# Performance work log

Hardware: AMD Instinct MI355X
Metric: run time of the kernel (lower is better)

## Reference

```python
import jax, jax.numpy as jnp
import numpy as np
from jax import lax

D_MODEL = 512
N_BLOCKS = 8
VOCAB = 2048
MEL = 80
D_INNER = 2 * D_MODEL      # standard Mamba expand=2
STATE = 16                 # AudioConstants.MAMBA_STATE_DIM
DT_RANK = D_MODEL // 16    # 32
CONV_K = 4                 # causal depthwise conv kernel
B, T = 4, 2048


def setup_inputs() -> dict:
    key = jax.random.key(0)
    ks = jax.random.split(key, 16)
    s = 0.02
    nb = N_BLOCKS
    inp = {
        "feats": jax.random.normal(ks[0], (B, T, MEL), jnp.float32),
        "feat_lens": jax.random.randint(ks[1], (B,), 0, T, jnp.int32),
        # frontend
        "conv1_w": jax.random.normal(ks[2], (D_MODEL, MEL, 3), jnp.float32) * s,
        "conv1_b": jnp.zeros((D_MODEL,), jnp.float32),
        "conv2_w": jax.random.normal(ks[3], (D_MODEL, D_MODEL, 3), jnp.float32) * s,
        "conv2_b": jnp.zeros((D_MODEL,), jnp.float32),
        # stacked per-block Mamba params (leading dim = n_blocks)
        "norm_w": jnp.ones((nb, D_MODEL), jnp.float32),
        "in_proj_w": jax.random.normal(ks[4], (nb, D_MODEL, 2 * D_INNER), jnp.float32) * s,
        "dwconv_w": jax.random.normal(ks[5], (nb, D_INNER, CONV_K), jnp.float32) * s,
        "dwconv_b": jnp.zeros((nb, D_INNER), jnp.float32),
        "x_proj_w": jax.random.normal(ks[6], (nb, D_INNER, DT_RANK + 2 * STATE), jnp.float32) * s,
        "dt_proj_w": jax.random.normal(ks[7], (nb, DT_RANK, D_INNER), jnp.float32) * s,
        "dt_proj_b": jnp.full((nb, D_INNER), -4.6, jnp.float32),  # softplus(-4.6)~0.01
        "A_log": jnp.tile(jnp.log(jnp.arange(1, STATE + 1, dtype=jnp.float32))[None, None, :], (nb, D_INNER, 1)),
        "Dskip": jnp.ones((nb, D_INNER), jnp.float32),
        "out_proj_w": jax.random.normal(ks[8], (nb, D_INNER, D_MODEL), jnp.float32) * s,
        # CTC head
        "head_w": jax.random.normal(ks[9], (D_MODEL, VOCAB), jnp.float32) * s,
        "head_b": jnp.zeros((VOCAB,), jnp.float32),
    }
    return inp


def _conv1d(x, w, b, stride, pad):
    # x: (B, Cin, L), w: (Cout, Cin, K)
    y = lax.conv_general_dilated(x, w, (stride,), [(pad, pad)],
                                 dimension_numbers=("NCH", "OIH", "NCH"))
    return y + b[None, :, None]


def _mamba_layer(x, p):
    nw, ipw, cw, cb, xpw, dpw, dpb, alog, dsk, opw = p
    res = x
    # RMSNorm
    xn = x * lax.rsqrt(jnp.mean(x * x, axis=-1, keepdims=True) + 1e-5) * nw
    xz = xn @ ipw                                # (B, L, 2*di)
    xs, z = jnp.split(xz, 2, axis=-1)
    # causal depthwise conv over time
    xc = jnp.pad(xs.transpose(0, 2, 1), ((0, 0), (0, 0), (CONV_K - 1, 0)))
    xc = lax.conv_general_dilated(xc, cw[:, None, :], (1,), [(0, 0)],
                                  dimension_numbers=("NCH", "OIH", "NCH"),
                                  feature_group_count=D_INNER)
    xs = jax.nn.silu((xc + cb[None, :, None]).transpose(0, 2, 1))  # (B, L, di)
    # input-dependent SSM params
    xdb = xs @ xpw                               # (B, L, dt_rank + 2N)
    dt, Bm, Cm = jnp.split(xdb, [DT_RANK, DT_RANK + STATE], axis=-1)
    delta = jax.nn.softplus(dt @ dpw + dpb)      # (B, L, di)
    A = -jnp.exp(alog)                           # (di, N)
    dA = jnp.exp(delta[..., None] * A)           # (B, L, di, N)
    dBx = delta[..., None] * Bm[:, :, None, :] * xs[..., None]

    def step(h, inp):
        dA_t, dBx_t, C_t = inp                   # (B,di,N),(B,di,N),(B,N)
        h = dA_t * h + dBx_t
        y = jnp.einsum("bdn,bn->bd", h, C_t)
        return h, y

    h0 = jnp.zeros((x.shape[0], D_INNER, STATE), x.dtype)
    _, ys = lax.scan(step, h0, (dA.transpose(1, 0, 2, 3),
                                dBx.transpose(1, 0, 2, 3),
                                Cm.transpose(1, 0, 2)))
    y = ys.transpose(1, 0, 2) + xs * dsk          # (B, L, di)
    y = y * jax.nn.silu(z)
    return res + y @ opw, None


def reference(feats, feat_lens, conv1_w, conv1_b, conv2_w, conv2_b,
              norm_w, in_proj_w, dwconv_w, dwconv_b, x_proj_w,
              dt_proj_w, dt_proj_b, A_log, Dskip, out_proj_w,
              head_w, head_b):
    x = feats.transpose(0, 2, 1)                  # (B, 80, T)
    x = jax.nn.gelu(_conv1d(x, conv1_w, conv1_b, 2, 1), approximate=False)
    x = jax.nn.gelu(_conv1d(x, conv2_w, conv2_b, 2, 1), approximate=False)
    x = x.transpose(0, 2, 1)                      # (B, T/4, D)
    params = (norm_w, in_proj_w, dwconv_w, dwconv_b, x_proj_w,
              dt_proj_w, dt_proj_b, A_log, Dskip, out_proj_w)
    x, _ = lax.scan(_mamba_layer, x, params)
    logits = x @ head_w + head_b                  # (B, T/4, V)
    out_lens = jnp.maximum(feat_lens // 4, 1)
    return logits, out_lens
```

## Files before the change

kernel.cpp:

```cpp
#include <hip/hip_runtime.h>
#include <hip/hip_bf16.h>

#define DMODEL 512
#define NB 8
#define VOCABSZ 2048
#define MEL 80
#define DIN 1024
#define NSTATE 16
#define DTRANK 32
#define BATCH 4
#define TIN 2048
#define LL1 1024
#define LSEQ 512
#define MROWS (BATCH*LSEQ)
#define M1ROWS (BATCH*LL1)
#define NCHUNK 16
#define LCHUNK 32

typedef unsigned short u16;
typedef unsigned int   u32;
typedef __attribute__((ext_vector_type(8))) short short8;
typedef __attribute__((ext_vector_type(4))) float f32x4;

__device__ __forceinline__ float bf2f(u16 v) { return __uint_as_float(((u32)v) << 16); }
__device__ __forceinline__ u16 f2bf(float f) {
    u32 u = __float_as_uint(f);
    return (u16)((u + 0x7fffu + ((u >> 16) & 1u)) >> 16);
}
__device__ __forceinline__ float gelu_exact(float v) {
    return 0.5f * v * (1.0f + erff(v * 0.70710678118654752f));
}
__device__ __forceinline__ float silu_f(float v) { return v / (1.0f + __expf(-v)); }
__device__ __forceinline__ float softplus_f(float v) { return v > 20.f ? v : log1pf(__expf(v)); }

template<int WM, int WN, int MR, int NR, int EPI, int SPLITK>
__global__ __launch_bounds__(WM*WN*64) void gemm2_bf16(
    const u16* __restrict__ A, int lda,
    const u16* __restrict__ BT, int ldb,
    const float* __restrict__ bias,
    float* __restrict__ Cf, u16* __restrict__ Cb, int ldc,
    int K, int zstride)
{
    constexpr int BM = WM * MR * 16;
    constexpr int BN = WN * NR * 16;
    constexpr int NT = WM * WN * 64;
    constexpr int LA = (BM * 4) / NT;
    constexpr int LB = (BN * 4) / NT;
    __shared__ __align__(16) u16 As[2][BM * 32];
    __shared__ __align__(16) u16 Bs[2][BN * 32];
    const int tid = threadIdx.x;
    const int m0 = blockIdx.y * BM, n0 = blockIdx.x * BN;
    const int lane = tid & 63;
    const int wave = tid >> 6;
    const int wm = wave / WN, wn = wave % WN;
    const int lr = lane & 15, lk = lane >> 4;

    int kt0 = 0, kend = K;
    if (SPLITK > 1) {
        const int kb = K / SPLITK;
        kt0 = blockIdx.z * kb;
        kend = kt0 + kb;
        Cf += (size_t)blockIdx.z * zstride;
    }

    f32x4 acc[MR][NR];
#pragma unroll
    for (int m = 0; m < MR; ++m)
#pragma unroll
        for (int n = 0; n < NR; ++n) acc[m][n] = (f32x4){0.f, 0.f, 0.f, 0.f};

    auto stage = [&](int buf, int kt) {
#pragma unroll
        for (int c = 0; c < LA; ++c) {
            int idx = c * NT + tid;
            const u16* src = A + (size_t)(m0 + (idx >> 2)) * lda + kt + (idx & 3) * 8;
            __builtin_amdgcn_global_load_lds(
                (const __attribute__((address_space(1))) void*)src,
                (__attribute__((address_space(3))) void*)&As[buf][idx * 8], 16, 0, 0);
        }
#pragma unroll
        for (int c = 0; c < LB; ++c) {
            int idx = c * NT + tid;
            const u16* src = BT + (size_t)(n0 + (idx >> 2)) * ldb + kt + (idx & 3) * 8;
            __builtin_amdgcn_global_load_lds(
                (const __attribute__((address_space(1))) void*)src,
                (__attribute__((address_space(3))) void*)&Bs[buf][idx * 8], 16, 0, 0);
        }
    };

    stage(0, kt0);
    __syncthreads();
    int cur = 0;
    for (int kt = kt0; kt < kend; kt += 32) {
        if (kt + 32 < kend) stage(cur ^ 1, kt + 32);
        short8 a[MR], b[NR];
#pragma unroll
        for (int m = 0; m < MR; ++m)
            a[m] = *(const short8*)&As[cur][((wm * MR + m) * 16 + lr) * 32 + lk * 8];
#pragma unroll
        for (int n = 0; n < NR; ++n)
            b[n] = *(const short8*)&Bs[cur][((wn * NR + n) * 16 + lr) * 32 + lk * 8];
#pragma unroll
        for (int m = 0; m < MR; ++m)
#pragma unroll
            for (int n = 0; n < NR; ++n)
                acc[m][n] = __builtin_amdgcn_mfma_f32_16x16x32_bf16(a[m], b[n], acc[m][n], 0, 0, 0);
        __syncthreads();
        cur ^= 1;
    }

#pragma unroll
    for (int m = 0; m < MR; ++m) {
#pragma unroll
        for (int n = 0; n < NR; ++n) {
#pragma unroll
            for (int r = 0; r < 4; ++r) {
                const int row = m0 + (wm * MR + m) * 16 + lk * 4 + r;
                const int col = n0 + (wn * NR + n) * 16 + lr;
                float v = acc[m][n][r];
                if (EPI == 1)      v += bias[col];
                else if (EPI == 2) v = gelu_exact(v + bias[col]);
                else if (EPI == 3) v = softplus_f(v + bias[col]);
                else if (EPI == 4) v += Cf[(size_t)row * ldc + col];
                if (Cf) Cf[(size_t)row * ldc + col] = v;
                if (Cb) Cb[(size_t)row * ldc + col] = f2bf(v);
            }
        }
    }
}

__global__ __launch_bounds__(256) void tcast_k(const float* __restrict__ in, u16* __restrict__ out,
                                               int R, int C, size_t sin, size_t sout) {
    in  += (size_t)blockIdx.z * sin;
    out += (size_t)blockIdx.z * sout;
    __shared__ float s[32][33];
    const int tx = threadIdx.x & 31, ty = threadIdx.x >> 5;
    const int r0 = blockIdx.y * 32, c0 = blockIdx.x * 32;
#pragma unroll
    for (int i = 0; i < 4; ++i)
        s[ty + i * 8][tx] = in[(size_t)(r0 + ty + i * 8) * C + c0 + tx];
    __syncthreads();
#pragma unroll
    for (int i = 0; i < 4; ++i)
        out[(size_t)(c0 + ty + i * 8) * R + r0 + tx] = f2bf(s[tx][ty + i * 8]);
}

__global__ void castpad_k(const float* __restrict__ in, u16* __restrict__ out,
                          int rows, int cin, int cout, int instride,
                          size_t sin, size_t sout) {
    in  += (size_t)blockIdx.z * sin;
    out += (size_t)blockIdx.z * sout;
    int idx = blockIdx.x * 256 + threadIdx.x;
    if (idx >= rows * cout) return;
    int c = idx % cout, r = idx / cout;
    out[idx] = (c < cin) ? f2bf(in[(size_t)r * instride + c]) : (u16)0;
}

__global__ void im2col1_k(const float* __restrict__ feats, u16* __restrict__ out) {
    int idx = blockIdx.x * 256 + threadIdx.x;
    int c = idx & 255, m = idx >> 8;
    int l1 = m & (LL1 - 1), b = m >> 10;
    float v = 0.f;
    if (c < 240) {
        int ci = c / 3, kk = c - ci * 3;
        int t = 2 * l1 - 1 + kk;
        if (t >= 0 && t < TIN) v = feats[((size_t)b * TIN + t) * MEL + ci];
    }
    out[idx] = f2bf(v);
}

__global__ void im2col2_k(const u16* __restrict__ y1b, u16* __restrict__ out) {
    int idx = blockIdx.x * 256 + threadIdx.x;
    int c = idx % 1536, m = idx / 1536;
    int l = m & (LSEQ - 1), b = m >> 9;
    int ci = c / 3, kk = c - ci * 3;
    int t = 2 * l - 1 + kk;
    out[idx] = (t >= 0 && t < LL1) ? y1b[((size_t)b * LL1 + t) * 512 + ci] : (u16)0;
}

__global__ __launch_bounds__(256) void rmsnorm_k(const float* __restrict__ x,
                                                 const float* __restrict__ nw,
                                                 u16* __restrict__ xn) {
    int m = blockIdx.x;
    int tid = threadIdx.x;
    const float2 v = *reinterpret_cast<const float2*>(&x[(size_t)m * DMODEL + tid * 2]);
    float ss = v.x * v.x + v.y * v.y;
#pragma unroll
    for (int o = 32; o > 0; o >>= 1) ss += __shfl_down(ss, o);
    __shared__ float sred[4];
    __shared__ float sscale;
    if ((tid & 63) == 0) sred[tid >> 6] = ss;
    __syncthreads();
    if (tid == 0) {
        float tot = sred[0] + sred[1] + sred[2] + sred[3];
        sscale = rsqrtf(tot / 512.f + 1e-5f);
    }
    __syncthreads();
    float sc = sscale;
    u32 pack = (u32)f2bf(v.x * sc * nw[tid * 2]) | ((u32)f2bf(v.y * sc * nw[tid * 2 + 1]) << 16);
    *reinterpret_cast<u32*>(&xn[(size_t)m * DMODEL + tid * 2]) = pack;
}

__global__ __launch_bounds__(256) void dwconv_silu_k(const u16* __restrict__ xzb,
                                                     const float* __restrict__ cw,
                                                     const float* __restrict__ cb,
                                                     u16* __restrict__ xsb) {
    int d = blockIdx.x * 256 + threadIdx.x;
    int m = blockIdx.y;
    int l = m & (LSEQ - 1);
    int b = m >> 9;
    float acc = cb[d];
    const float4 w4 = *reinterpret_cast<const float4*>(&cw[d * 4]);
    const float wk[4] = {w4.x, w4.y, w4.z, w4.w};
#pragma unroll
    for (int k = 0; k < 4; k++) {
        int t = l - 3 + k;
        if (t >= 0) acc += wk[k] * bf2f(xzb[((size_t)(b * LSEQ + t)) * (2 * DIN) + d]);
    }
    xsb[(size_t)m * DIN + d] = f2bf(silu_f(acc));
}

__global__ void xreduce_k(const float* __restrict__ part, float* __restrict__ xdb,
                          u16* __restrict__ dtb) {
    int i4 = blockIdx.x * 256 + threadIdx.x;
    const float4 p0 = *(const float4*)&part[i4 * 4];
    const float4 p1 = *(const float4*)&part[131072 + i4 * 4];
    const float4 p2 = *(const float4*)&part[262144 + i4 * 4];
    const float4 p3 = *(const float4*)&part[393216 + i4 * 4];
    float4 s;
    s.x = p0.x + p1.x + p2.x + p3.x;
    s.y = p0.y + p1.y + p2.y + p3.y;
    s.z = p0.z + p1.z + p2.z + p3.z;
    s.w = p0.w + p1.w + p2.w + p3.w;
    *(float4*)&xdb[i4 * 4] = s;
    int c4 = i4 & 15, r = i4 >> 4;
    if (c4 < 8) {
        u32 lo = (u32)f2bf(s.x) | ((u32)f2bf(s.y) << 16);
        u32 hi = (u32)f2bf(s.z) | ((u32)f2bf(s.w) << 16);
        *(u32*)&dtb[r * 32 + c4 * 4]     = lo;
        *(u32*)&dtb[r * 32 + c4 * 4 + 2] = hi;
    }
}

template<int PASS>
__global__ __launch_bounds__(256) void scan_chunk_k(
    const u16* __restrict__ deltab, const u16* __restrict__ xsb,
    const float* __restrict__ xdb, const u16* __restrict__ xzb,
    const float* __restrict__ alog, const float* __restrict__ dsk,
    float* __restrict__ P, float* __restrict__ Q,
    u16* __restrict__ yb)
{
    __shared__ float s_bc[LCHUNK * 32];
    __shared__ float s_dl[LCHUNK * 64];
    __shared__ float s_xs[LCHUNK * 64];
    __shared__ float s_z [PASS ? LCHUNK * 64 : 1];

    const int tid  = threadIdx.x;
    const int j    = tid & 3;
    const int dsub = tid >> 2;
    const int d0   = blockIdx.x * 64;
    const int c    = blockIdx.y;
    const int b    = blockIdx.z;
    const int d    = d0 + dsub;
    const size_t rbase = (size_t)b * LSEQ + c * LCHUNK;

    for (int idx = tid; idx < LCHUNK * 32; idx += 256) {
        int t = idx >> 5, cc = idx & 31;
        s_bc[idx] = xdb[(rbase + t) * 64 + 32 + cc];
    }
    for (int idx = tid; idx < LCHUNK * 64; idx += 256) {
        int t = idx >> 6, dd = idx & 63;
        s_dl[idx] = bf2f(deltab[(rbase + t) * DIN + d0 + dd]);
        s_xs[idx] = bf2f(xsb[(rbase + t) * DIN + d0 + dd]);
        if (PASS) s_z[idx] = bf2f(xzb[(rbase + t) * (2 * DIN) + DIN + d0 + dd]);
    }
    __syncthreads();

    float a[4], h[4];
#pragma unroll
    for (int nj = 0; nj < 4; nj++)
        a[nj] = -__expf(alog[(size_t)d * NSTATE + j * 4 + nj]);

    const size_t chstride = (size_t)DIN * NSTATE;
    const size_t chcol = (size_t)d * NSTATE + j * 4;
    h[0] = h[1] = h[2] = h[3] = 0.f;
    if (PASS) {
        for (int c2 = 0; c2 < c; ++c2) {
            const size_t o = ((size_t)(b * NCHUNK + c2)) * chstride + chcol;
            const float4 Pv = *(const float4*)&P[o];
            const float4 Qv = *(const float4*)&Q[o];
            h[0] = fmaf(Pv.x, h[0], Qv.x);
            h[1] = fmaf(Pv.y, h[1], Qv.y);
            h[2] = fmaf(Pv.z, h[2], Qv.z);
            h[3] = fmaf(Pv.w, h[3], Qv.w);
        }
    }
    const float dskv = PASS ? dsk[d] : 0.f;
    float sdl = 0.f;

    for (int t = 0; t < LCHUNK; t++) {
        const float dl = s_dl[t * 64 + dsub];
        const float xv = s_xs[t * 64 + dsub];
        const float dlx = dl * xv;
        if (!PASS) sdl += dl;
        float yv = 0.f;
#pragma unroll
        for (int nj = 0; nj < 4; nj++) {
            const float bn = s_bc[t * 32 + j * 4 + nj];
            const float dA = __expf(dl * a[nj]);
            h[nj] = fmaf(dA, h[nj], dlx * bn);
            if (PASS) {
                const float cn = s_bc[t * 32 + 16 + j * 4 + nj];
                yv = fmaf(h[nj], cn, yv);
            }
        }
        if (PASS) {
            yv += __shfl_xor(yv, 1);
            yv += __shfl_xor(yv, 2);
            if (j == 0) {
                const float zv = s_z[t * 64 + dsub];
                yb[(rbase + t) * DIN + d] = f2bf((yv + xv * dskv) * silu_f(zv));
            }
        }
    }

    if (!PASS) {
        const size_t o = ((size_t)(b * NCHUNK + c)) * chstride + chcol;
        float4 Pv, Qv;
        Pv.x = __expf(a[0] * sdl); Pv.y = __expf(a[1] * sdl);
        Pv.z = __expf(a[2] * sdl); Pv.w = __expf(a[3] * sdl);
        Qv.x = h[0]; Qv.y = h[1]; Qv.z = h[2]; Qv.w = h[3];
        *(float4*)&P[o] = Pv;
        *(float4*)&Q[o] = Qv;
    }
}

__global__ void lens_k(const int* __restrict__ feat_lens, float* __restrict__ out) {
    int b = threadIdx.x;
    if (b < BATCH) {
        int v = feat_lens[b] / 4;
        if (v < 1) v = 1;
        out[b] = (float)v;
    }
}

extern "C" void kernel_launch(void* const* d_in, const int* in_sizes, int n_in,
                              void* d_out, int out_size, void* d_ws, size_t ws_size,
                              hipStream_t stream)
{
    const float* feats = (const float*)d_in[0];
    const int*   flens = (const int*)  d_in[1];
    const float* c1w = (const float*)d_in[2];
    const float* c1b = (const float*)d_in[3];
    const float* c2w = (const float*)d_in[4];
    const float* c2b = (const float*)d_in[5];
    const float* nw  = (const float*)d_in[6];
    const float* ipw = (const float*)d_in[7];
    const float* cw  = (const float*)d_in[8];
    const float* cb  = (const float*)d_in[9];
    const float* xpw = (const float*)d_in[10];
    const float* dpw = (const float*)d_in[11];
    const float* dpb = (const float*)d_in[12];
    const float* alog= (const float*)d_in[13];
    const float* dskp= (const float*)d_in[14];
    const float* opw = (const float*)d_in[15];
    const float* hw  = (const float*)d_in[16];
    const float* hb  = (const float*)d_in[17];

    float* ws = (float*)d_ws;
    u16*  XZb    = (u16*)ws;
    float* X     = ws + 2097152;
    u16*  XN     = (u16*)(ws + 3145728);
    u16*  Xb     = (u16*)(ws + 3670016);
    u16*  XSb    = (u16*)(ws + 4194304);
    u16*  DELb   = (u16*)(ws + 5242880);
    float* XDB   = ws + 6291456;
    float* P     = ws + 6422528;
    u16*  dtb    = (u16*)(ws + 7471104);
    u16*  Yb     = (u16*)(ws + 7503872);
    float* XDBp  = ws + 8552448;
    u16*  ipwTa  = (u16*)(ws + 9076736);
    u16*  opwTa  = (u16*)(ws + 13271040);
    u16*  hwT    = (u16*)(ws + 15368192);
    u16*  xpwT   = (u16*)(ws + 15892480);
    u16*  dpwT   = (u16*)(ws + 16154624);
    u16*  c1wb   = (u16*)(ws + 16285696);
    u16*  c2wb   = (u16*)(ws + 16351232);
    u16*  Y1b    = (u16*)(ws + 16744448);
    float* logits = (float*)d_out;
    float* Q     = logits;

    castpad_k<<<dim3(512, 1, 1), 256, 0, stream>>>(c1w, c1wb, 512, 240, 256, 240, 0, 0);
    castpad_k<<<dim3(3072, 1, 1), 256, 0, stream>>>(c2w, c2wb, 512, 1536, 1536, 1536, 0, 0);
    tcast_k<<<dim3(64, 16, 1), 256, 0, stream>>>(hw, hwT, 512, 2048, 0, 0);
    tcast_k<<<dim3(2, 32, 8), 256, 0, stream>>>(xpw, xpwT, 1024, 64, 65536, 65536);
    tcast_k<<<dim3(32, 1, 8), 256, 0, stream>>>(dpw, dpwT, 32, 1024, 32768, 32768);
    tcast_k<<<dim3(64, 16, 8), 256, 0, stream>>>(ipw, ipwTa, 512, 2048, 1048576, 1048576);
    tcast_k<<<dim3(16, 32, 8), 256, 0, stream>>>(opw, opwTa, 1024, 512, 524288, 524288);

    im2col1_k<<<4096, 256, 0, stream>>>(feats, XZb);
    gemm2_bf16<2, 2, 4, 2, 2, 1><<<dim3(8, 32), 256, 0, stream>>>(
        XZb, 256, c1wb, 256, c1b, nullptr, Y1b, 512, 256, 0);
    im2col2_k<<<12288, 256, 0, stream>>>(Y1b, XZb);
    gemm2_bf16<2, 2, 2, 2, 2, 1><<<dim3(8, 32), 256, 0, stream>>>(
        XZb, 1536, c2wb, 1536, c2b, X, nullptr, 512, 1536, 0);

    for (int blk = 0; blk < NB; ++blk) {
        rmsnorm_k<<<MROWS, 256, 0, stream>>>(X, nw + blk * DMODEL, XN);
        gemm2_bf16<2, 2, 4, 2, 0, 1><<<dim3(32, 16), 256, 0, stream>>>(
            XN, 512, ipwTa + (size_t)blk * 1048576, 512, nullptr,
            nullptr, XZb, 2048, 512, 0);
        dwconv_silu_k<<<dim3(4, MROWS), 256, 0, stream>>>(
            XZb, cw + blk * DIN * 4, cb + blk * DIN, XSb);
        gemm2_bf16<2, 2, 2, 2, 0, 4><<<dim3(1, 32, 4), 256, 0, stream>>>(
            XSb, 1024, xpwT + (size_t)blk * 65536, 1024, nullptr,
            XDBp, nullptr, 64, 1024, 131072);
        xreduce_k<<<128, 256, 0, stream>>>(XDBp, XDB, dtb);
        gemm2_bf16<2, 2, 4, 2, 3, 1><<<dim3(16, 16), 256, 0, stream>>>(
            dtb, 32, dpwT + (size_t)blk * 32768, 32, dpb + blk * DIN,
            nullptr, DELb, 1024, 32, 0);
        scan_chunk_k<0><<<dim3(16, NCHUNK, BATCH), 256, 0, stream>>>(
            DELb, XSb, XDB, nullptr, alog + (size_t)blk * DIN * NSTATE,
            nullptr, P, Q, nullptr);
        scan_chunk_k<1><<<dim3(16, NCHUNK, BATCH), 256, 0, stream>>>(
            DELb, XSb, XDB, XZb, alog + (size_t)blk * DIN * NSTATE,
            dskp + blk * DIN, P, Q, Yb);
        gemm2_bf16<2, 2, 2, 2, 4, 1><<<dim3(8, 32), 256, 0, stream>>>(
            Yb, 1024, opwTa + (size_t)blk * 524288, 1024, nullptr,
            X, Xb, 512, 1024, 0);
    }

    gemm2_bf16<2, 2, 4, 2, 1, 1><<<dim3(32, 16), 256, 0, stream>>>(
        Xb, 512, hwT, 512, hb, logits, nullptr, 2048, 512, 0);
    lens_k<<<1, 64, 0, stream>>>(flens, logits + (size_t)MROWS * VOCABSZ);
}
```

Baseline: 858.6 us.

## Fold RMSNorm weight into in_proj and apply row scale in GEMM epilogue

RMSNorm is split so the per-channel weight is multiplied into the transposed in_proj weights once, and the per-row rsqrt scale is applied in the GEMM epilogue. A small row-scale kernel replaces the normalized bf16 activation write, and the GEMM reads the bf16 copy of X the previous out_proj GEMM already produces. The scan chunking changes from 16x32 to 32x16, and the lens kernel is merged into im2col1. Applying the scale after accumulation instead of before bf16 rounding slightly changes numerics.

Measured after the change: 885.1 us. 1.03x slower.

```diff
diff --git a/kernel.cpp b/kernel.cpp
--- a/kernel.cpp
+++ b/kernel.cpp
@@ -7,15 +7,14 @@
 #define MEL 80
 #define DIN 1024
 #define NSTATE 16
-#define DTRANK 32
 #define BATCH 4
 #define TIN 2048
 #define LL1 1024
 #define LSEQ 512
 #define MROWS (BATCH*LSEQ)
 #define M1ROWS (BATCH*LL1)
-#define NCHUNK 16
-#define LCHUNK 32
+#define NCHUNK 32
+#define LCHUNK 16
 
 typedef unsigned short u16;
 typedef unsigned int   u32;
@@ -122,6 +121,7 @@
                 else if (EPI == 2) v = gelu_exact(v + bias[col]);
                 else if (EPI == 3) v = softplus_f(v + bias[col]);
                 else if (EPI == 4) v += Cf[(size_t)row * ldc + col];
+                else if (EPI == 6) v *= bias[row];
                 if (Cf) Cf[(size_t)row * ldc + col] = v;
                 if (Cb) Cb[(size_t)row * ldc + col] = f2bf(v);
             }
@@ -143,6 +143,25 @@
 #pragma unroll
     for (int i = 0; i < 4; ++i)
         out[(size_t)(c0 + ty + i * 8) * R + r0 + tx] = f2bf(s[tx][ty + i * 8]);
+}
+
+__global__ __launch_bounds__(256) void tcast_nw_k(const float* __restrict__ in, u16* __restrict__ out,
+                                                  const float* __restrict__ nwp,
+                                                  int R, int C, size_t sin, size_t sout, int nws) {
+    in  += (size_t)blockIdx.z * sin;
+    out += (size_t)blockIdx.z * sout;
+    nwp += (size_t)blockIdx.z * nws;
+    __shared__ float s[32][33];
+    const int tx = threadIdx.x & 31, ty = threadIdx.x >> 5;
+    const int r0 = blockIdx.y * 32, c0 = blockIdx.x * 32;
+#pragma unroll
+    for (int i = 0; i < 4; ++i)
+        s[ty + i * 8][tx] = in[(size_t)(r0 + ty + i * 8) * C + c0 + tx];
+    __syncthreads();
+    const float nwv = nwp[r0 + tx];
+#pragma unroll
+    for (int i = 0; i < 4; ++i)
+        out[(size_t)(c0 + ty + i * 8) * R + r0 + tx] = f2bf(s[tx][ty + i * 8] * nwv);
 }
 
 __global__ void castpad_k(const float* __restrict__ in, u16* __restrict__ out,
@@ -156,8 +175,14 @@
     out[idx] = (c < cin) ? f2bf(in[(size_t)r * instride + c]) : (u16)0;
 }
 
-__global__ void im2col1_k(const float* __restrict__ feats, u16* __restrict__ out) {
+__global__ void im2col1_k(const float* __restrict__ feats, u16* __restrict__ out,
+                          const int* __restrict__ feat_lens, float* __restrict__ lens_out) {
     int idx = blockIdx.x * 256 + threadIdx.x;
+    if (blockIdx.x == 0 && threadIdx.x < BATCH) {
+        int v = feat_lens[threadIdx.x] / 4;
+        if (v < 1) v = 1;
+        lens_out[threadIdx.x] = (float)v;
+    }
     int c = idx & 255, m = idx >> 8;
     int l1 = m & (LL1 - 1), b = m >> 10;
     float v = 0.f;
@@ -178,27 +203,17 @@
     out[idx] = (t >= 0 && t < LL1) ? y1b[((size_t)b * LL1 + t) * 512 + ci] : (u16)0;
 }
 
-__global__ __launch_bounds__(256) void rmsnorm_k(const float* __restrict__ x,
-                                                 const float* __restrict__ nw,
-                                                 u16* __restrict__ xn) {
-    int m = blockIdx.x;
-    int tid = threadIdx.x;
-    const float2 v = *reinterpret_cast<const float2*>(&x[(size_t)m * DMODEL + tid * 2]);
-    float ss = v.x * v.x + v.y * v.y;
-#pragma unroll
-    for (int o = 32; o > 0; o >>= 1) ss += __shfl_down(ss, o);
-    __shared__ float sred[4];
-    __shared__ float sscale;
-    if ((tid & 63) == 0) sred[tid >> 6] = ss;
-    __syncthreads();
-    if (tid == 0) {
-        float tot = sred[0] + sred[1] + sred[2] + sred[3];
-        sscale = rsqrtf(tot / 512.f + 1e-5f);
-    }
-    __syncthreads();
-    float sc = sscale;
-    u32 pack = (u32)f2bf(v.x * sc * nw[tid * 2]) | ((u32)f2bf(v.y * sc * nw[tid * 2 + 1]) << 16);
-    *reinterpret_cast<u32*>(&xn[(size_t)m * DMODEL + tid * 2]) = pack;
+__global__ __launch_bounds__(256) void rowsc_k(const float* __restrict__ X,
+                                               float* __restrict__ scrow) {
+    const int lane = threadIdx.x & 63;
+    const int row = blockIdx.x * 4 + (threadIdx.x >> 6);
+    const float4 v0 = *(const float4*)&X[(size_t)row * 512 + lane * 8];
+    const float4 v1 = *(const float4*)&X[(size_t)row * 512 + lane * 8 + 4];
+    float ss = v0.x * v0.x + v0.y * v0.y + v0.z * v0.z + v0.w * v0.w
+             + v1.x * v1.x + v1.y * v1.y + v1.z * v1.z + v1.w * v1.w;
+#pragma unroll
+    for (int o = 1; o < 64; o <<= 1) ss += __shfl_xor(ss, o);
+    if (lane == 0) scrow[row] = rsqrtf(ss * (1.f / 512.f) + 1e-5f);
 }
 
 __global__ __launch_bounds__(256) void dwconv_silu_k(const u16* __restrict__ xzb,
@@ -332,15 +347,6 @@
         Qv.x = h[0]; Qv.y = h[1]; Qv.z = h[2]; Qv.w = h[3];
         *(float4*)&P[o] = Pv;
         *(float4*)&Q[o] = Qv;
-    }
-}
-
-__global__ void lens_k(const int* __restrict__ feat_lens, float* __restrict__ out) {
-    int b = threadIdx.x;
-    if (b < BATCH) {
-        int v = feat_lens[b] / 4;
-        if (v < 1) v = 1;
-        out[b] = (float)v;
     }
 }
 
@@ -370,23 +376,23 @@
     float* ws = (float*)d_ws;
     u16*  XZb    = (u16*)ws;
     float* X     = ws + 2097152;
-    u16*  XN     = (u16*)(ws + 3145728);
-    u16*  Xb     = (u16*)(ws + 3670016);
+    u16*  Xb     = (u16*)(ws + 3145728);
+    float* scrow = ws + 3670016;
     u16*  XSb    = (u16*)(ws + 4194304);
     u16*  DELb   = (u16*)(ws + 5242880);
     float* XDB   = ws + 6291456;
-    float* P     = ws + 6422528;
-    u16*  dtb    = (u16*)(ws + 7471104);
-    u16*  Yb     = (u16*)(ws + 7503872);
-    float* XDBp  = ws + 8552448;
-    u16*  ipwTa  = (u16*)(ws + 9076736);
-    u16*  opwTa  = (u16*)(ws + 13271040);
-    u16*  hwT    = (u16*)(ws + 15368192);
-    u16*  xpwT   = (u16*)(ws + 15892480);
-    u16*  dpwT   = (u16*)(ws + 16154624);
-    u16*  c1wb   = (u16*)(ws + 16285696);
-    u16*  c2wb   = (u16*)(ws + 16351232);
-    u16*  Y1b    = (u16*)(ws + 16744448);
+    u16*  dtb    = (u16*)(ws + 6422528);
+    float* P     = ws + 6455296;
+    u16*  Yb     = (u16*)(ws + 8552448);
+    float* XDBp  = ws + 9601024;
+    u16*  ipwTa  = (u16*)(ws + 10125312);
+    u16*  opwTa  = (u16*)(ws + 14319616);
+    u16*  hwT    = (u16*)(ws + 16416768);
+    u16*  xpwT   = (u16*)(ws + 16941056);
+    u16*  dpwT   = (u16*)(ws + 17203200);
+    u16*  c1wb   = (u16*)(ws + 17334272);
+    u16*  c2wb   = (u16*)(ws + 17399808);
+    u16*  Y1b    = XSb;
     float* logits = (float*)d_out;
     float* Q     = logits;
 
@@ -395,20 +401,21 @@
     tcast_k<<<dim3(64, 16, 1), 256, 0, stream>>>(hw, hwT, 512, 2048, 0, 0);
     tcast_k<<<dim3(2, 32, 8), 256, 0, stream>>>(xpw, xpwT, 1024, 64, 65536, 65536);
     tcast_k<<<dim3(32, 1, 8), 256, 0, stream>>>(dpw, dpwT, 32, 1024, 32768, 32768);
-    tcast_k<<<dim3(64, 16, 8), 256, 0, stream>>>(ipw, ipwTa, 512, 2048, 1048576, 1048576);
+    tcast_nw_k<<<dim3(64, 16, 8), 256, 0, stream>>>(ipw, ipwTa, nw, 512, 2048,
+                                                    1048576, 1048576, DMODEL);
     tcast_k<<<dim3(16, 32, 8), 256, 0, stream>>>(opw, opwTa, 1024, 512, 524288, 524288);
 
-    im2col1_k<<<4096, 256, 0, stream>>>(feats, XZb);
+    im2col1_k<<<4096, 256, 0, stream>>>(feats, XZb, flens, logits + (size_t)MROWS * VOCABSZ);
     gemm2_bf16<2, 2, 4, 2, 2, 1><<<dim3(8, 32), 256, 0, stream>>>(
         XZb, 256, c1wb, 256, c1b, nullptr, Y1b, 512, 256, 0);
     im2col2_k<<<12288, 256, 0, stream>>>(Y1b, XZb);
     gemm2_bf16<2, 2, 2, 2, 2, 1><<<dim3(8, 32), 256, 0, stream>>>(
-        XZb, 1536, c2wb, 1536, c2b, X, nullptr, 512, 1536, 0);
+        XZb, 1536, c2wb, 1536, c2b, X, Xb, 512, 1536, 0);
 
     for (int blk = 0; blk < NB; ++blk) {
-        rmsnorm_k<<<MROWS, 256, 0, stream>>>(X, nw + blk * DMODEL, XN);
-        gemm2_bf16<2, 2, 4, 2, 0, 1><<<dim3(32, 16), 256, 0, stream>>>(
-            XN, 512, ipwTa + (size_t)blk * 1048576, 512, nullptr,
+        rowsc_k<<<512, 256, 0, stream>>>(X, scrow);
+        gemm2_bf16<2, 2, 4, 2, 6, 1><<<dim3(32, 16), 256, 0, stream>>>(
+            Xb, 512, ipwTa + (size_t)blk * 1048576, 512, scrow,
             nullptr, XZb, 2048, 512, 0);
         dwconv_silu_k<<<dim3(4, MROWS), 256, 0, stream>>>(
             XZb, cw + blk * DIN * 4, cb + blk * DIN, XSb);
@@ -432,5 +439,4 @@
 
     gemm2_bf16<2, 2, 4, 2, 1, 1><<<dim3(32, 16), 256, 0, stream>>>(
         Xb, 512, hwT, 512, hb, logits, nullptr, 2048, 512, 0);
-    lens_k<<<1, 64, 0, stream>>>(flens, logits + (size_t)MROWS * VOCABSZ);
-}
+}
```
